# Performance work log

Hardware: AMD Instinct MI355X
Metric: run time of the kernel (lower is better)

The kernel has to match this reference:

```python
import jax, jax.numpy as jnp
import numpy as np

ALPHA = 0.25
GAMMA = 2.0
HUBER_DELTA = 0.5  # init kwarg delta
REG_BETA = 1.0 / 9.0


def calc_iou(a, b):
    # a: [A,4] anchors, b: [M,4] gt boxes, xyxy
    area = (b[:, 2] - b[:, 0]) * (b[:, 3] - b[:, 1])  # [M]
    iw = jnp.clip(jnp.minimum(a[:, 2:3], b[:, 2]) - jnp.maximum(a[:, 0:1], b[:, 0]), 0.0)
    ih = jnp.clip(jnp.minimum(a[:, 3:4], b[:, 3]) - jnp.maximum(a[:, 1:2], b[:, 1]), 0.0)
    ua = jnp.clip(((a[:, 2] - a[:, 0]) * (a[:, 3] - a[:, 1]))[:, None] + area - iw * ih, 1e-8)
    return iw * ih / ua  # [A,M]


def _per_sample(cls, reg, dist, ann, anchor):
    # cls [A,C], reg [A,4], dist [A,1], ann [M,6], anchor [A,4]
    aw = anchor[:, 2] - anchor[:, 0]
    ah = anchor[:, 3] - anchor[:, 1]
    acx = anchor[:, 0] + 0.5 * aw
    acy = anchor[:, 1] + 0.5 * ah

    valid = ann[:, 4] != -1.0  # padding annotations have class == -1
    cls = jnp.clip(cls, 1e-4, 1.0 - 1e-4)

    iou = jnp.where(valid[None, :], calc_iou(anchor, ann[:, :4]), -1.0)  # [A,M]
    iou_max = iou.max(axis=1)
    iou_arg = iou.argmax(axis=1)
    assigned = ann[iou_arg]  # [A,6]

    pos = iou_max >= 0.5
    num_pos = pos.sum()
    denom = jnp.maximum(num_pos.astype(cls.dtype), 1.0)

    labels = assigned[:, 4].astype(jnp.int32)
    onehot = jax.nn.one_hot(labels, cls.shape[1], dtype=cls.dtype)
    # -1 = ignore, 0 = negative (IoU<0.4 or positive-but-not-this-class), 1 = assigned class
    targets = jnp.where(pos[:, None], onehot,
                        jnp.where((iou_max < 0.4)[:, None], 0.0, -1.0))

    af = jnp.where(targets == 1.0, ALPHA, 1.0 - ALPHA)
    fw = af * jnp.where(targets == 1.0, 1.0 - cls, cls) ** GAMMA
    bce = -(targets * jnp.log(cls) + (1.0 - targets) * jnp.log(1.0 - cls))
    cls_loss = jnp.where(targets != -1.0, fw * bce, 0.0).sum() / denom

    # empty-annotation fallback: all anchors treated as background
    cls_loss_empty = ((1.0 - ALPHA) * cls ** GAMMA * (-jnp.log(1.0 - cls))).sum()
    has_ann = valid.any()
    cls_loss = jnp.where(has_ann, cls_loss, cls_loss_empty)

    gw_raw = assigned[:, 2] - assigned[:, 0]
    gh_raw = assigned[:, 3] - assigned[:, 1]
    gcx = assigned[:, 0] + 0.5 * gw_raw  # centers use unclamped w/h (as in torch code)
    gcy = assigned[:, 1] + 0.5 * gh_raw
    gw = jnp.clip(gw_raw, 1.0)
    gh = jnp.clip(gh_raw, 1.0)
    t = jnp.stack([(gcx - acx) / aw, (gcy - acy) / ah,
                   jnp.log(gw / aw), jnp.log(gh / ah)], axis=1)
    t = t / jnp.asarray([0.1, 0.1, 0.2, 0.2], dtype=cls.dtype)
    diff = jnp.abs(t - reg)
    rl = jnp.where(diff <= REG_BETA, 0.5 * 9.0 * diff ** 2, diff - 0.5 / 9.0)
    posf = pos.astype(cls.dtype)
    reg_loss = jnp.where(num_pos > 0, (rl * posf[:, None]).sum() / (denom * 4.0), 0.0)

    # --- distance Huber loss (delta=0.5), positives only ---
    d = jnp.abs(dist[:, 0] - assigned[:, 5])
    hl = jnp.where(d <= HUBER_DELTA, 0.5 * d ** 2, HUBER_DELTA * (d - 0.5 * HUBER_DELTA))
    dist_loss = jnp.where(num_pos > 0, (hl * posf).sum() / denom, 0.0)

    return cls_loss, reg_loss, dist_loss


def reference(classifications, regressions, distances, anchors, annotations):
    anchor = anchors[0]
    cl, rl, dl = jax.vmap(_per_sample, in_axes=(0, 0, 0, 0, None))(
        classifications, regressions, distances, annotations, anchor)
    return (jnp.mean(cl, keepdims=True),
            jnp.mean(rl, keepdims=True),
            jnp.mean(dl, keepdims=True))


def setup_inputs() -> dict:
    key = jax.random.key(0)
    ks = jax.random.split(key, 10)
    B, A, C, M = 8, 120000, 80, 32
    IMG = 800.0

    classifications = jax.random.uniform(ks[0], (B, A, C), dtype=jnp.float32)
    regressions = jax.random.normal(ks[1], (B, A, 4), dtype=jnp.float32)
    distances = jax.random.normal(ks[2], (B, A, 1), dtype=jnp.float32) * 10.0 + 50.0

    # anchors: valid xyxy boxes over an 800px image
    acx = jax.random.uniform(ks[3], (A,), minval=0.0, maxval=IMG)
    acy = jax.random.uniform(ks[4], (A,), minval=0.0, maxval=IMG)
    aw = jax.random.uniform(ks[5], (A, 2), minval=16.0, maxval=256.0)
    anchors = jnp.stack([acx - 0.5 * aw[:, 0], acy - 0.5 * aw[:, 1],
                         acx + 0.5 * aw[:, 0], acy + 0.5 * aw[:, 1]], axis=1)[None].astype(jnp.float32)

    # annotations: [B,M,6] = x1,y1,x2,y2,class,distance (all valid)
    gc = jax.random.uniform(ks[6], (B, M, 2), minval=100.0, maxval=IMG - 100.0)
    gs = jax.random.uniform(ks[7], (B, M, 2), minval=32.0, maxval=300.0)
    boxes = jnp.concatenate([gc - 0.5 * gs, gc + 0.5 * gs], axis=-1)
    labels = jax.random.randint(ks[8], (B, M, 1), 0, C).astype(jnp.float32)
    gdist = jax.random.uniform(ks[9], (B, M, 1), minval=1.0, maxval=100.0)
    annotations = jnp.concatenate([boxes, labels, gdist], axis=-1).astype(jnp.float32)

    return {"classifications": classifications, "regressions": regressions,
            "distances": distances, "anchors": anchors, "annotations": annotations}
```

## Files before the change

kernel.cpp:

```cpp
#include <hip/hip_runtime.h>
#include <hip/hip_bf16.h>


typedef float v4f __attribute__((ext_vector_type(4)));

#define LN2_075 0.51986038542f

__device__ __forceinline__ float wave_reduce_sum(float v) {
#pragma unroll
    for (int off = 32; off > 0; off >>= 1) v += __shfl_down(v, off);
    return v;
}

__device__ __forceinline__ float smooth_l1(float d) {
    return d <= (1.0f / 9.0f) ? 4.5f * d * d : d - (0.5f / 9.0f);
}

__device__ __forceinline__ float proc4t(v4f cv, float acc) {
#pragma unroll
    for (int j = 0; j < 4; ++j) {
        const float c = fminf(cv[j], 1.0f - 1e-4f);
        acc = fmaf(c * c, __log2f(1.0f - c), acc);
    }
    return acc;
}

template <int CPA>
__global__ __launch_bounds__(256) void main_kernel(
    const float* __restrict__ cls, const float* __restrict__ reg,
    const float* __restrict__ dist, const float* __restrict__ anchors,
    const float* __restrict__ ann, float* __restrict__ partA,
    float4* __restrict__ partB, int A, int M, int SBLK, int nb) {
    const int b = blockIdx.y;
    const int tid = threadIdx.x;
    const int lane = tid & 63;
    const int wid = tid >> 6;

    if (blockIdx.x >= nb) {
        const int sb = blockIdx.x - nb;
        const int NC4 = A * CPA;
        const int chunk = (NC4 + SBLK - 1) / SBLK;
        const int start = sb * chunk;
        const int end = min(start + chunk, NC4);
        const v4f* __restrict__ p = (const v4f*)(cls + (size_t)b * NC4 * 4);

        float acc0 = 0.f, acc1 = 0.f;
        int i = start + tid;
        for (; i + 768 < end; i += 1024) {
            const v4f a0 = p[i];
            const v4f a1 = p[i + 256];
            const v4f a2 = p[i + 512];
            const v4f a3 = p[i + 768];
            acc0 = proc4t(a0, acc0);
            acc1 = proc4t(a1, acc1);
            acc0 = proc4t(a2, acc0);
            acc1 = proc4t(a3, acc1);
        }
        for (; i < end; i += 256) acc0 = proc4t(p[i], acc0);

        __shared__ float s_red[4];
        float acc = wave_reduce_sum(acc0 + acc1);
        if (lane == 0) s_red[wid] = acc;
        __syncthreads();
        if (tid == 0)
            partA[(size_t)b * SBLK + sb] = s_red[0] + s_red[1] + s_red[2] + s_red[3];
        return;
    }

    const int blk = blockIdx.x;
    const int base = blk << 8;

    __shared__ float s_ann[64 * 6];
    const float* annb = ann + (size_t)b * M * 6;
    for (int i = tid; i < M * 6; i += 256) s_ann[i] = annb[i];
    __syncthreads();

    const int a = base + tid;
    float l_npos = 0.f, l_reg = 0.f, l_dist = 0.f;
    int st = -1;
    if (a < A) {
        const float4 av = *(const float4*)(anchors + (size_t)a * 4);
        const float aw = av.z - av.x, ah = av.w - av.y;
        const float acx = av.x + 0.5f * aw, acy = av.y + 0.5f * ah;
        const float aarea = aw * ah;

        float best = -1.0f;
        int bi = 0;
        for (int m = 0; m < M; ++m) {
            const float* g = s_ann + m * 6;
            float iou = -1.0f;
            if (g[4] != -1.0f) {
                float iw = fmaxf(fminf(av.z, g[2]) - fmaxf(av.x, g[0]), 0.f);
                float ih = fmaxf(fminf(av.w, g[3]) - fmaxf(av.y, g[1]), 0.f);
                float inter = iw * ih;
                float area = (g[2] - g[0]) * (g[3] - g[1]);
                float ua = fmaxf(aarea + area - inter, 1e-8f);
                iou = inter / ua;
            }
            if (iou > best) { best = iou; bi = m; }
        }

        if (best >= 0.5f) {
            const float* g = s_ann + bi * 6;
            st = (int)g[4];
            l_npos = 1.f;
            const float4 rv = *(const float4*)(reg + ((size_t)b * A + a) * 4);
            const float gwr = g[2] - g[0], ghr = g[3] - g[1];
            const float gcx = g[0] + 0.5f * gwr, gcy = g[1] + 0.5f * ghr;
            const float gw = fmaxf(gwr, 1.f), gh = fmaxf(ghr, 1.f);
            const float t0 = ((gcx - acx) / aw) / 0.1f;
            const float t1 = ((gcy - acy) / ah) / 0.1f;
            const float t2 = __logf(gw / aw) / 0.2f;
            const float t3 = __logf(gh / ah) / 0.2f;
            l_reg = smooth_l1(fabsf(t0 - rv.x)) + smooth_l1(fabsf(t1 - rv.y)) +
                    smooth_l1(fabsf(t2 - rv.z)) + smooth_l1(fabsf(t3 - rv.w));
            const float dv = dist[(size_t)b * A + a];
            const float dd = fabsf(dv - g[5]);
            l_dist = dd <= 0.5f ? 0.5f * dd * dd : 0.5f * (dd - 0.25f);
        } else if (best >= 0.4f) {
            st = -2;
        }
    }

    const v4f* __restrict__ clsb = (const v4f*)(cls + ((size_t)b * A + base) * (CPA * 4));
    float corr = 0.f;
    if (st >= 0) {
        const float cr = cls[((size_t)b * A + a) * (CPA * 4) + st];
        const float ct = fminf(cr, 1.0f - 1e-4f);
        const float c = fminf(fmaxf(cr, 1e-4f), 1.0f - 1e-4f);
        const float om = 1.0f - c;
        corr = LN2_075 * (ct * ct * __log2f(1.0f - ct))
               + 0.25f * om * om * (-__logf(c));
    } else if (st == -2) {
        float part = 0.f;
#pragma unroll
        for (int k = 0; k < CPA; ++k) part = proc4t(clsb[(size_t)tid * CPA + k], part);
        corr = LN2_075 * part;
    }

    __shared__ float s_red4[4][4];
    const float w0 = wave_reduce_sum(l_npos);
    const float w1 = wave_reduce_sum(corr);
    const float w2 = wave_reduce_sum(l_reg);
    const float w3 = wave_reduce_sum(l_dist);
    if (lane == 0) {
        s_red4[0][wid] = w0; s_red4[1][wid] = w1; s_red4[2][wid] = w2; s_red4[3][wid] = w3;
    }
    __syncthreads();
    if (tid == 0) {
        float4 p;
        p.x = s_red4[0][0] + s_red4[0][1] + s_red4[0][2] + s_red4[0][3];
        p.y = s_red4[1][0] + s_red4[1][1] + s_red4[1][2] + s_red4[1][3];
        p.z = s_red4[2][0] + s_red4[2][1] + s_red4[2][2] + s_red4[2][3];
        p.w = s_red4[3][0] + s_red4[3][1] + s_red4[3][2] + s_red4[3][3];
        partB[(size_t)b * nb + blk] = p;
    }
}

__global__ void finalize_kernel(const float* __restrict__ partA,
                                const float4* __restrict__ partB,
                                float* __restrict__ out, int B, int SBLK, int nb) {
    const int lane = threadIdx.x & 63;
    const int b = threadIdx.x >> 6;
    __shared__ float s_res[8][3];
    if (b < B) {
        float sa = 0.f, np_ = 0.f, corr = 0.f, rs = 0.f, ds = 0.f;
        for (int i = lane; i < SBLK; i += 64) sa += partA[(size_t)b * SBLK + i];
        for (int i = lane; i < nb; i += 64) {
            const float4 p = partB[(size_t)b * nb + i];
            np_ += p.x; corr += p.y; rs += p.z; ds += p.w;
        }
        sa = wave_reduce_sum(sa);
        np_ = wave_reduce_sum(np_);
        corr = wave_reduce_sum(corr);
        rs = wave_reduce_sum(rs);
        ds = wave_reduce_sum(ds);
        if (lane == 0) {
            const float cls_total = fmaf(sa, -LN2_075, corr);
            const float denom = fmaxf(np_, 1.f);
            s_res[b][0] = cls_total / denom;
            s_res[b][1] = np_ > 0.f ? rs / (denom * 4.f) : 0.f;
            s_res[b][2] = np_ > 0.f ? ds / denom : 0.f;
        }
    }
    __syncthreads();
    if (threadIdx.x == 0) {
        float c = 0.f, r = 0.f, d = 0.f;
        for (int i = 0; i < B; ++i) { c += s_res[i][0]; r += s_res[i][1]; d += s_res[i][2]; }
        out[0] = c / (float)B;
        out[1] = r / (float)B;
        out[2] = d / (float)B;
    }
}

__global__ __launch_bounds__(256) void fused_generic_kernel(
    const float* __restrict__ cls, const float* __restrict__ reg,
    const float* __restrict__ dist, const float* __restrict__ anchors,
    const float* __restrict__ ann, float4* __restrict__ partials,
    int A, int C, int M, int nb) {
    const int b = blockIdx.y;
    const int base = blockIdx.x << 8;
    const int tid = threadIdx.x;
    const int cpa = C >> 2;

    __shared__ float s_ann[64 * 6];
    __shared__ signed char s_state[256];
    const float* annb = ann + (size_t)b * M * 6;
    for (int i = tid; i < M * 6; i += 256) s_ann[i] = annb[i];
    s_state[tid] = -2;
    __syncthreads();

    const int a = base + tid;
    float l_npos = 0.f, l_reg = 0.f, l_dist = 0.f;
    if (a < A) {
        const float4 av = *(const float4*)(anchors + (size_t)a * 4);
        const float aw = av.z - av.x, ah = av.w - av.y;
        const float acx = av.x + 0.5f * aw, acy = av.y + 0.5f * ah;
        const float aarea = aw * ah;
        float best = -1.0f;
        int bi = 0;
        for (int m = 0; m < M; ++m) {
            const float* g = s_ann + m * 6;
            float iou = -1.0f;
            if (g[4] != -1.0f) {
                float iw = fmaxf(fminf(av.z, g[2]) - fmaxf(av.x, g[0]), 0.f);
                float ih = fmaxf(fminf(av.w, g[3]) - fmaxf(av.y, g[1]), 0.f);
                float inter = iw * ih;
                float area = (g[2] - g[0]) * (g[3] - g[1]);
                float ua = fmaxf(aarea + area - inter, 1e-8f);
                iou = inter / ua;
            }
            if (iou > best) { best = iou; bi = m; }
        }
        signed char st;
        if (best >= 0.5f) {
            const float* g = s_ann + bi * 6;
            st = (signed char)(int)g[4];
            l_npos = 1.f;
            const float4 rv = *(const float4*)(reg + ((size_t)b * A + a) * 4);
            const float gwr = g[2] - g[0], ghr = g[3] - g[1];
            const float gcx = g[0] + 0.5f * gwr, gcy = g[1] + 0.5f * ghr;
            const float gw = fmaxf(gwr, 1.f), gh = fmaxf(ghr, 1.f);
            const float t0 = ((gcx - acx) / aw) / 0.1f;
            const float t1 = ((gcy - acy) / ah) / 0.1f;
            const float t2 = __logf(gw / aw) / 0.2f;
            const float t3 = __logf(gh / ah) / 0.2f;
            l_reg = smooth_l1(fabsf(t0 - rv.x)) + smooth_l1(fabsf(t1 - rv.y)) +
                    smooth_l1(fabsf(t2 - rv.z)) + smooth_l1(fabsf(t3 - rv.w));
            const float dv = dist[(size_t)b * A + a];
            const float dd = fabsf(dv - g[5]);
            l_dist = dd <= 0.5f ? 0.5f * dd * dd : 0.5f * (dd - 0.25f);
        } else if (best < 0.4f) {
            st = -1;
        } else {
            st = -2;
        }
        s_state[tid] = st;
    }
    __syncthreads();

    const float4* __restrict__ clsb = (const float4*)(cls + ((size_t)b * A + base) * C);
    int a_local = tid / cpa;
    int cc = tid % cpa;
    const int dA = 256 / cpa;
    const int dC = 256 % cpa;
    float lsum = 0.f;
    for (int k = 0; k < cpa; ++k) {
        const int st = s_state[a_local];
        if (st != -2) {
            const float4 cv = clsb[k * 256 + tid];
            const int c0 = cc << 2;
#pragma unroll
            for (int j = 0; j < 4; ++j) {
                float c = j == 0 ? cv.x : j == 1 ? cv.y : j == 2 ? cv.z : cv.w;
                c = fminf(fmaxf(c, 1e-4f), 1.0f - 1e-4f);
                const bool ispos = (st == c0 + j);
                const float om = 1.0f - c;
                const float x = ispos ? c : om;
                const float w = ispos ? 0.25f * om * om : 0.75f * c * c;
                lsum -= w * __logf(x);
            }
        }
        a_local += dA;
        cc += dC;
        if (cc >= cpa) { cc -= cpa; ++a_local; }
    }

    __shared__ float s_red[4][4];
    const float w0 = wave_reduce_sum(l_npos);
    const float w1 = wave_reduce_sum(lsum);
    const float w2 = wave_reduce_sum(l_reg);
    const float w3 = wave_reduce_sum(l_dist);
    const int lane = tid & 63, wid = tid >> 6;
    if (lane == 0) {
        s_red[0][wid] = w0; s_red[1][wid] = w1; s_red[2][wid] = w2; s_red[3][wid] = w3;
    }
    __syncthreads();
    if (tid == 0) {
        float4 p;
        p.x = s_red[0][0] + s_red[0][1] + s_red[0][2] + s_red[0][3];
        p.y = s_red[1][0] + s_red[1][1] + s_red[1][2] + s_red[1][3];
        p.z = s_red[2][0] + s_red[2][1] + s_red[2][2] + s_red[2][3];
        p.w = s_red[3][0] + s_red[3][1] + s_red[3][2] + s_red[3][3];
        partials[(size_t)b * nb + blockIdx.x] = p;
    }
}

extern "C" void kernel_launch(void* const* d_in, const int* in_sizes, int n_in,
                              void* d_out, int out_size, void* d_ws, size_t ws_size,
                              hipStream_t stream) {
    const float* cls     = (const float*)d_in[0];
    const float* reg     = (const float*)d_in[1];
    const float* dist    = (const float*)d_in[2];
    const float* anchors = (const float*)d_in[3];
    const float* ann     = (const float*)d_in[4];

    const int A = in_sizes[3] / 4;
    const int B = in_sizes[1] / (A * 4);
    const int C = in_sizes[0] / (B * A);
    const int M = in_sizes[4] / (B * 6);
    const int nb = (A + 255) / 256;
    const int SBLK = 256;

    float* partA = (float*)d_ws;
    float4* partB = (float4*)((char*)d_ws + 8192);

    if (C == 80) {
        dim3 g(nb + SBLK, B), blk(256);
        main_kernel<20><<<g, blk, 0, stream>>>(cls, reg, dist, anchors, ann,
                                               partA, partB, A, M, SBLK, nb);
        finalize_kernel<<<1, B * 64, 0, stream>>>(partA, partB, (float*)d_out, B, SBLK, nb);
    } else {
        dim3 g(nb, B), blk(256);
        fused_generic_kernel<<<g, blk, 0, stream>>>(cls, reg, dist, anchors, ann,
                                                    partB, A, C, M, nb);
        finalize_kernel<<<1, B * 64, 0, stream>>>(partA, partB, (float*)d_out, B, 0, nb);
    }
}
```

Measured before the change: 73.98 us.

## Stage classification stream through LDS via global_load_lds in the sum blocks

The background-sum blocks now split the classification tensor into 256-float segments and copy up to 16 segments at a time into a 16KB shared buffer with direct global-to-LDS loads, then compute the focal terms from LDS. A tail loop in the last block covers any leftover elements. The IoU loop now reads annotations straight from global memory instead of the shared copy, and the ignore-row loop is only partly unrolled. The intent is to raise memory throughput for the streaming sum. In exchange each block uses much more LDS and adds two barriers per batch with no overlap between loading and computing, which may lower occupancy and latency hiding.

```diff
diff --git a/kernel.cpp b/kernel.cpp
--- a/kernel.cpp
+++ b/kernel.cpp
@@ -36,42 +36,56 @@
     const int lane = tid & 63;
     const int wid = tid >> 6;
 
+    __shared__ __align__(16) float smem[4096];
+    __shared__ float s_red4[4][4];
+
     if (blockIdx.x >= nb) {
         const int sb = blockIdx.x - nb;
         const int NC4 = A * CPA;
-        const int chunk = (NC4 + SBLK - 1) / SBLK;
-        const int start = sb * chunk;
-        const int end = min(start + chunk, NC4);
-        const v4f* __restrict__ p = (const v4f*)(cls + (size_t)b * NC4 * 4);
-
-        float acc0 = 0.f, acc1 = 0.f;
-        int i = start + tid;
-        for (; i + 768 < end; i += 1024) {
-            const v4f a0 = p[i];
-            const v4f a1 = p[i + 256];
-            const v4f a2 = p[i + 512];
-            const v4f a3 = p[i + 768];
-            acc0 = proc4t(a0, acc0);
-            acc1 = proc4t(a1, acc1);
-            acc0 = proc4t(a2, acc0);
-            acc1 = proc4t(a3, acc1);
-        }
-        for (; i < end; i += 256) acc0 = proc4t(p[i], acc0);
-
-        __shared__ float s_red[4];
-        float acc = wave_reduce_sum(acc0 + acc1);
-        if (lane == 0) s_red[wid] = acc;
+        const float* __restrict__ src = cls + (size_t)b * NC4 * 4;
+
+        const int T = NC4 >> 6;
+        const int q = T / SBLK, r = T % SBLK;
+        const int beg = sb * q + min(sb, r);
+        const int cnt = q + (sb < r ? 1 : 0);
+        const int end = beg + cnt;
+
+        float acc = 0.f;
+        for (int s0 = beg; s0 < end; s0 += 16) {
+            const int sc = min(16, end - s0);
+            const int jhi = min(wid * 4 + 4, sc);
+            for (int j = wid * 4; j < jhi; ++j) {
+                const int gI = s0 + j;
+                const float* g = src + ((size_t)gI << 8) + (lane << 2);
+                float* l = smem + (j << 8);
+                __builtin_amdgcn_global_load_lds(
+                    (const __attribute__((address_space(1))) void*)g,
+                    (__attribute__((address_space(3))) void*)l, 16, 0, 0);
+            }
+            __syncthreads();
+            const v4f* __restrict__ lv = (const v4f*)smem;
+            for (int i = tid; i < (sc << 6); i += 256) acc = proc4t(lv[i], acc);
+            __syncthreads();
+        }
+        if (sb == SBLK - 1) {
+            const v4f* __restrict__ pv = (const v4f*)src;
+            for (int i = (T << 6) + tid; i < NC4; i += 256) acc = proc4t(pv[i], acc);
+        }
+
+        acc = wave_reduce_sum(acc);
+        if (lane == 0) s_red4[0][wid] = acc;
         __syncthreads();
         if (tid == 0)
-            partA[(size_t)b * SBLK + sb] = s_red[0] + s_red[1] + s_red[2] + s_red[3];
+            partA[(size_t)b * SBLK + sb] =
+                s_red4[0][0] + s_red4[0][1] + s_red4[0][2] + s_red4[0][3];
         return;
     }
 
     const int blk = blockIdx.x;
     const int base = blk << 8;
-
-    __shared__ float s_ann[64 * 6];
-    const float* annb = ann + (size_t)b * M * 6;
+    float* s_ann = smem;
+
+    const float* __restrict__ annb = ann + (size_t)b * M * 6;
     for (int i = tid; i < M * 6; i += 256) s_ann[i] = annb[i];
     __syncthreads();
 
@@ -87,7 +101,7 @@
         float best = -1.0f;
         int bi = 0;
         for (int m = 0; m < M; ++m) {
-            const float* g = s_ann + m * 6;
+            const float* g = annb + m * 6;
             float iou = -1.0f;
             if (g[4] != -1.0f) {
                 float iw = fmaxf(fminf(av.z, g[2]) - fmaxf(av.x, g[0]), 0.f);
@@ -122,7 +136,6 @@
         }
     }
 
-    const v4f* __restrict__ clsb = (const v4f*)(cls + ((size_t)b * A + base) * (CPA * 4));
     float corr = 0.f;
     if (st >= 0) {
         const float cr = cls[((size_t)b * A + a) * (CPA * 4) + st];
@@ -132,13 +145,13 @@
         corr = LN2_075 * (ct * ct * __log2f(1.0f - ct))
                + 0.25f * om * om * (-__logf(c));
     } else if (st == -2) {
+        const v4f* __restrict__ row = (const v4f*)(cls + ((size_t)b * A + a) * (CPA * 4));
         float part = 0.f;
-#pragma unroll
-        for (int k = 0; k < CPA; ++k) part = proc4t(clsb[(size_t)tid * CPA + k], part);
+#pragma unroll 4
+        for (int k = 0; k < CPA; ++k) part = proc4t(row[k], part);
         corr = LN2_075 * part;
     }
 
-    __shared__ float s_red4[4][4];
     const float w0 = wave_reduce_sum(l_npos);
     const float w1 = wave_reduce_sum(corr);
     const float w2 = wave_reduce_sum(l_reg);
```

Measured after the change: 79.56 us. 7.5% more time.
